# Kernel optimization log

Measured on AMD Instinct MI355X. Metric: run time of the kernel, lower is better.

Reference implementation:

```python
import jax, jax.numpy as jnp
import numpy as np

N, R, A, F = 6000, 5, 8, 128
K, O = 2, 128
RADIUS = 0.028
ROT_DELTA = 1


def _kernel_matrix(n_radial, n_angular, radius):
    # polar grid of kernel vertices -> cartesian, shape (R, A, 2)
    r = radius * (np.arange(1, n_radial + 1, dtype=np.float64) / n_radial)
    theta = 2.0 * np.pi * np.arange(n_angular, dtype=np.float64) / n_angular
    x = r[:, None] * np.cos(theta)[None, :]
    y = r[:, None] * np.sin(theta)[None, :]
    return np.stack([x, y], axis=-1)


def _interp_coefficients(n_radial, n_angular, radius):
    # Gaussian interpolation weights w(rho_a,theta_b,rho_c,theta_d), normalized,
    # reshaped to (R, A, R*A) as in _configure_patch_operator.
    kv = _kernel_matrix(n_radial, n_angular, radius)           # (R, A, 2)
    flat = kv.reshape(-1, 2)                                   # (R*A, 2)
    d2 = ((kv[:, :, None, :] - flat[None, None, :, :]) ** 2).sum(-1)  # (R, A, R*A)
    sigma = radius / n_radial
    w = np.exp(-d2 / (2.0 * sigma * sigma))
    w = w / w.sum(axis=-1, keepdims=True)
    return w.astype(np.float32)


def setup_inputs() -> dict:
    key = jax.random.key(0)
    k1, k2, k3, k4, k5 = jax.random.split(key, 5)
    mesh_signal = jax.random.normal(k1, (N, F), dtype=jnp.float32)
    # barycentric coords: channel 0 = vertex indices (stored as float), channel 1 = weights summing to 1
    idx = jax.random.randint(k2, (N, R, A, 3), 0, N).astype(jnp.float32)
    w = jax.random.uniform(k3, (N, R, A, 3), dtype=jnp.float32)
    w = w / w.sum(axis=-1, keepdims=True)
    bary_coordinates = jnp.stack([idx, w], axis=-1)            # (N, R, A, 3, 2)
    kernel_weights = jax.random.normal(k4, (R, A, K, O, F), dtype=jnp.float32) * 0.05
    bias = jax.random.normal(k5, (K, O), dtype=jnp.float32) * 0.05
    interp_coeffs = jnp.asarray(_interp_coefficients(R, A, RADIUS))  # (R, A, R*A)
    return {"mesh_signal": mesh_signal, "bary_coordinates": bary_coordinates,
            "kernel_weights": kernel_weights, "bias": bias, "interp_coeffs": interp_coeffs}


def reference(mesh_signal, bary_coordinates, kernel_weights, bias, interp_coeffs):
    # 1) gather + barycentric interpolation
    idx = bary_coordinates[..., 0].astype(jnp.int32)           # (N, R, A, 3)
    w = bary_coordinates[..., 1]                               # (N, R, A, 3)
    collected = mesh_signal[idx]                               # (N, R, A, 3, F)
    sig = jnp.sum(w[..., None] * collected, axis=-2)           # (N, R, A, F)
    # 2) patch operator: F_x @ I[a,b]
    flat = sig.reshape(-1, R * A, F)                           # (N, R*A, F)
    patched = jnp.einsum('nqf,raq->nraf', flat, interp_coeffs)  # (N, R, A, F)
    # 3) rotation-shifted fold (splits=1 -> single chunk; splits don't change math)
    outs = []
    for rot in range(0, A, ROT_DELTA):
        rolled = jnp.roll(patched, shift=rot, axis=2)          # (N, R, A, F)
        s = jnp.einsum('nraf,rakof->nko', rolled, kernel_weights) + (R * A) * bias  # (N, K, O)
        outs.append(jax.nn.relu(s).sum(axis=1))                # (N, O)
    return jnp.stack(outs, axis=1)                             # (N, n_rotations, O)
```

## Files before the change

### kernel.cpp

```cpp
#include <hip/hip_runtime.h>
#include <hip/hip_bf16.h>


#define N_PTS 6000
#define RR 5
#define AA 8
#define FF 128
#define OO 128
#define QQ 40
#define KD2 1280
#define SIG_BLOCKS 750
#define W2_BLOCKS 128
#define CCQ 0.70710678118654752f
#define RT2 1.41421356237309515f

#define AHS ((size_t)N_PTS * KD2)
#define BHS ((size_t)512 * KD2)

typedef __bf16 bf16_t;
typedef __bf16 bf16x2 __attribute__((ext_vector_type(2)));
typedef __bf16 bf16x8 __attribute__((ext_vector_type(8)));
typedef float f32x4 __attribute__((ext_vector_type(4)));

#define GLOAD_LDS16(g, l)                                              \
  __builtin_amdgcn_global_load_lds(                                    \
      (const __attribute__((address_space(1))) void*)(g),              \
      (__attribute__((address_space(3))) void*)(l), 16, 0, 0)

#define DFT8V(xx, c, X0, X4, Xr1, Xi1, Xr2, Xi2, Xr3, Xi3)             \
  {                                                                    \
    const float s0_ = xx[0][c] + xx[4][c], s1_ = xx[1][c] + xx[5][c];  \
    const float s2_ = xx[2][c] + xx[6][c], s3_ = xx[3][c] + xx[7][c];  \
    const float d0_ = xx[0][c] - xx[4][c], d1_ = xx[1][c] - xx[5][c];  \
    const float d2_ = xx[2][c] - xx[6][c], d3_ = xx[3][c] - xx[7][c];  \
    const float e_ = CCQ * (d1_ - d3_), o_ = CCQ * (d1_ + d3_);        \
    X0 = (s0_ + s2_) + (s1_ + s3_);                                    \
    X4 = (s0_ + s2_) - (s1_ + s3_);                                    \
    Xr2 = s0_ - s2_; Xi2 = s3_ - s1_;                                  \
    Xr1 = d0_ + e_;  Xi1 = -(o_ + d2_);                                \
    Xr3 = d0_ - e_;  Xi3 = d2_ - o_;                                   \
  }

#define PACKP(dst, P, Q)                                               \
  {                                                                    \
    bf16x8 pv_;                                                        \
    pv_[0] = (bf16_t)P[0]; pv_[1] = (bf16_t)Q[0];                      \
    pv_[2] = (bf16_t)P[1]; pv_[3] = (bf16_t)Q[1];                      \
    pv_[4] = (bf16_t)P[2]; pv_[5] = (bf16_t)Q[2];                      \
    pv_[6] = (bf16_t)P[3]; pv_[7] = (bf16_t)Q[3];                      \
    *(bf16x8*)(dst) = pv_;                                             \
  }

__global__ __launch_bounds__(256, 6) void prep_fft_kernel(
    const float* __restrict__ mesh, const float* __restrict__ bary,
    const float* __restrict__ kw, const float* __restrict__ interp,
    bf16_t* __restrict__ Ahat, bf16_t* __restrict__ Bhat) {
  __shared__ float sh[1920];
  const int bx = blockIdx.x;
  const int tid = threadIdx.x;

  if (bx < SIG_BLOCKS) {
    const int slot = tid >> 5;
    const int l = tid & 31;
    const int n = bx * 8 + slot;
    const float* bbase = bary + (size_t)bx * 8 * (QQ * 6);
    for (int i = tid; i < 1920; i += 256) sh[i] = bbase[i];
    __syncthreads();
    const float* bp = sh + slot * 240;
    bf16_t* an = Ahat + (size_t)n * KD2 + l * 8;
#pragma unroll
    for (int rho = 0; rho < RR; ++rho) {
      float x[8][4];
#pragma unroll
      for (int a = 0; a < 8; ++a) {
        const float* rec = bp + (rho * 8 + a) * 6;
        const float2 p0 = *(const float2*)(rec);
        const float2 p1 = *(const float2*)(rec + 2);
        const float2 p2 = *(const float2*)(rec + 4);
        const float4 v0 =
            *(const float4*)(mesh + (size_t)((int)p0.x) * FF + l * 4);
        const float4 v1 =
            *(const float4*)(mesh + (size_t)((int)p1.x) * FF + l * 4);
        const float4 v2 =
            *(const float4*)(mesh + (size_t)((int)p2.x) * FF + l * 4);
        x[a][0] = p0.y * v0.x + p1.y * v1.x + p2.y * v2.x;
        x[a][1] = p0.y * v0.y + p1.y * v1.y + p2.y * v2.y;
        x[a][2] = p0.y * v0.z + p1.y * v1.z + p2.y * v2.z;
        x[a][3] = p0.y * v0.w + p1.y * v1.w + p2.y * v2.w;
      }
      float X0[4], X4[4], Xr1[4], Xi1[4], Xr2[4], Xi2[4], Xr3[4], Xi3[4];
#pragma unroll
      for (int c = 0; c < 4; ++c)
        DFT8V(x, c, X0[c], X4[c], Xr1[c], Xi1[c], Xr2[c], Xi2[c], Xr3[c],
              Xi3[c]);
      bf16_t* dst = an + rho * 256;
      PACKP(dst, X0, X4);
      PACKP(dst + AHS, Xr1, Xi1);
      PACKP(dst + 2 * AHS, Xr2, Xi2);
      PACKP(dst + 3 * AHS, Xr3, Xi3);
    }
  } else {
    const int j = (bx - SIG_BLOCKS) * 2 + (tid >> 7);
    const int f = tid & 127;
    for (int i = tid; i < RR * AA * QQ; i += 256) sh[i] = interp[i];
    __syncthreads();
    const int o = (j >> 1) & 127;
    const int k = j & 1;
    float acc[QQ];
#pragma unroll
    for (int q = 0; q < QQ; ++q) acc[q] = 0.f;
    for (int r = 0; r < RR; ++r) {
      for (int a = 0; a < AA; ++a) {
        const float kv =
            kw[((size_t)((r * AA + a) * 2 + k) * OO + o) * FF + f];
        const float4* ip = (const float4*)(sh + (r * AA + a) * QQ);
#pragma unroll
        for (int q4 = 0; q4 < QQ / 4; ++q4) {
          const float4 w4 = ip[q4];
          acc[q4 * 4 + 0] += w4.x * kv;
          acc[q4 * 4 + 1] += w4.y * kv;
          acc[q4 * 4 + 2] += w4.z * kv;
          acc[q4 * 4 + 3] += w4.w * kv;
        }
      }
    }
    const float SC = 0.125f;
    bf16_t* b1p = Bhat + (size_t)j * KD2;
    bf16_t* b2p = Bhat + (size_t)(256 + j) * KD2;
#pragma unroll
    for (int rho = 0; rho < RR; ++rho) {
      float xx[8][1];
#pragma unroll
      for (int a = 0; a < 8; ++a) xx[a][0] = acc[rho * 8 + a];
      float Y0, Y4, Yr1, Yi1, Yr2, Yi2, Yr3, Yi3;
      DFT8V(xx, 0, Y0, Y4, Yr1, Yi1, Yr2, Yi2, Yr3, Yi3);
      const int off = rho * 256 + f * 2;
      bf16x2 w;
      w[0] = (bf16_t)(Y0 * SC);   w[1] = (bf16_t)0.f;
      *(bf16x2*)(b1p + off) = w;
      w[0] = (bf16_t)0.f;         w[1] = (bf16_t)(Y4 * SC);
      *(bf16x2*)(b2p + off) = w;
      w[0] = (bf16_t)(Yr1 * SC);  w[1] = (bf16_t)(Yi1 * SC);
      *(bf16x2*)(b1p + BHS + off) = w;
      w[0] = (bf16_t)(Yi1 * SC);  w[1] = (bf16_t)(-Yr1 * SC);
      *(bf16x2*)(b2p + BHS + off) = w;
      w[0] = (bf16_t)(Yr2 * SC);  w[1] = (bf16_t)(Yi2 * SC);
      *(bf16x2*)(b1p + 2 * BHS + off) = w;
      w[0] = (bf16_t)(Yi2 * SC);  w[1] = (bf16_t)(-Yr2 * SC);
      *(bf16x2*)(b2p + 2 * BHS + off) = w;
      w[0] = (bf16_t)(Yr3 * SC);  w[1] = (bf16_t)(Yi3 * SC);
      *(bf16x2*)(b1p + 3 * BHS + off) = w;
      w[0] = (bf16_t)(Yi3 * SC);  w[1] = (bf16_t)(-Yr3 * SC);
      *(bf16x2*)(b2p + 3 * BHS + off) = w;
    }
  }
}

__global__ __launch_bounds__(256, 3) void gemm_fused_fft_kernel(
    const bf16_t* __restrict__ Ahat, const bf16_t* __restrict__ Bhat,
    const float* __restrict__ bias, float* __restrict__ out) {
  const int L = blockIdx.x;
  const int xcd = L & 7;
  const int t = L >> 3;
  const int g = xcd + 8 * (t >> 4);
  const int jt = t & 15;
  const int m0 = g * 128;
  if (m0 >= N_PTS) return;
  const int j0 = jt * 16;

  __shared__ bf16_t As[128 * 64];
  __shared__ bf16_t Bs[32 * 64];
  const int tid = threadIdx.x;
  const int wave = tid >> 6;
  const int lane = tid & 63;
  const int quad = lane >> 4;
  const int tl = lane & 15;
  const int wm = wave * 32;
  const int srow = lane >> 3;
  const int sc = (lane & 7) ^ srow;

  const int crow = wave * 8;
  const int colbase = (crow < 16) ? (j0 + crow) : (256 + j0 + (crow - 16));
  const int gcol = colbase + srow;

  static const float CF[4][8] = {
      {1, 1, 1, 1, 1, 1, 1, 1},
      {2, RT2, 0, -RT2, -2, -RT2, 0, RT2},
      {2, 0, -2, 0, 2, 0, -2, 0},
      {2, -RT2, 0, RT2, -2, RT2, 0, -RT2}};
  static const float SF[4][8] = {
      {1, -1, 1, -1, 1, -1, 1, -1},
      {0, -RT2, -2, -RT2, 0, RT2, 2, RT2},
      {0, -2, 0, 2, 0, -2, 0, 2},
      {0, -RT2, 2, -RT2, 0, RT2, -2, RT2}};

  f32x4 oacc[8][2];
#pragma unroll
  for (int rot = 0; rot < 8; ++rot)
#pragma unroll
    for (int mm = 0; mm < 2; ++mm) oacc[rot][mm] = {0.f, 0.f, 0.f, 0.f};

#pragma unroll
  for (int b = 0; b < 4; ++b) {
    const bf16_t* A = Ahat + (size_t)b * AHS;
    const bf16_t* B = Bhat + (size_t)b * BHS;
    f32x4 z[2][2];
#pragma unroll
    for (int mm = 0; mm < 2; ++mm)
#pragma unroll
      for (int cc = 0; cc < 2; ++cc) z[mm][cc] = {0.f, 0.f, 0.f, 0.f};

    for (int kk = 0; kk < KD2; kk += 64) {
      __syncthreads();
#pragma unroll
      for (int i = 0; i < 4; ++i) {
        const int row = wave * 32 + i * 8;
        int gm = m0 + row + srow;
        gm = gm < N_PTS ? gm : (N_PTS - 1);
        GLOAD_LDS16(A + (size_t)gm * KD2 + kk + sc * 8, As + row * 64);
      }
      GLOAD_LDS16(B + (size_t)gcol * KD2 + kk + sc * 8, Bs + crow * 64);
      __syncthreads();
#pragma unroll
      for (int ks = 0; ks < 2; ++ks) {
        const int ch = (((ks * 4 + quad) ^ (tl & 7)) * 8);
        bf16x8 af[2], bfr[2];
        af[0] = *(const bf16x8*)(As + (wm + tl) * 64 + ch);
        af[1] = *(const bf16x8*)(As + (wm + 16 + tl) * 64 + ch);
        bfr[0] = *(const bf16x8*)(Bs + tl * 64 + ch);
        bfr[1] = *(const bf16x8*)(Bs + (16 + tl) * 64 + ch);
#pragma unroll
        for (int mm = 0; mm < 2; ++mm)
#pragma unroll
          for (int cc = 0; cc < 2; ++cc)
            z[mm][cc] = __builtin_amdgcn_mfma_f32_16x16x32_bf16(
                af[mm], bfr[cc], z[mm][cc], 0, 0, 0);
      }
    }
#pragma unroll
    for (int rot = 0; rot < 8; ++rot) {
      const float cf = CF[b][rot], sf = SF[b][rot];
#pragma unroll
      for (int mm = 0; mm < 2; ++mm)
#pragma unroll
        for (int r = 0; r < 4; ++r)
          oacc[rot][mm][r] += cf * z[mm][0][r] + sf * z[mm][1][r];
    }
  }

  const int j = j0 + tl;
  const float bb = 40.0f * bias[((j & 1) << 7) | (j >> 1)];
  const int o = j >> 1;
#pragma unroll
  for (int rot = 0; rot < 8; ++rot)
#pragma unroll
    for (int mm = 0; mm < 2; ++mm)
#pragma unroll
      for (int r = 0; r < 4; ++r) {
        const int mrow = m0 + wm + mm * 16 + quad * 4 + r;
        float v = oacc[rot][mm][r] + bb;
        v = v > 0.f ? v : 0.f;
        const float vs = v + __shfl_xor(v, 1, 64);
        if (((lane & 1) == 0) && (mrow < N_PTS))
          out[(size_t)mrow * 1024 + rot * 128 + o] = vs;
      }
}

extern "C" void kernel_launch(void* const* d_in, const int* in_sizes, int n_in,
                              void* d_out, int out_size, void* d_ws,
                              size_t ws_size, hipStream_t stream) {
  const float* mesh = (const float*)d_in[0];
  const float* bary = (const float*)d_in[1];
  const float* kw = (const float*)d_in[2];
  const float* bias = (const float*)d_in[3];
  const float* interp = (const float*)d_in[4];
  float* out = (float*)d_out;

  bf16_t* Ahat = (bf16_t*)d_ws;
  bf16_t* Bhat = (bf16_t*)((char*)d_ws + 4 * AHS * 2);

  prep_fft_kernel<<<SIG_BLOCKS + W2_BLOCKS, 256, 0, stream>>>(
      mesh, bary, kw, interp, Ahat, Bhat);
  gemm_fused_fft_kernel<<<768, 256, 0, stream>>>(Ahat, Bhat, bias, out);
}
```

Before: 165.6 us.

## Store A operand in MFMA-fragment-native layout and load it directly to registers

```diff
diff --git a/kernel.cpp b/kernel.cpp
--- a/kernel.cpp
+++ b/kernel.cpp
@@ -67,7 +67,9 @@
     for (int i = tid; i < 1920; i += 256) sh[i] = bbase[i];
     __syncthreads();
     const float* bp = sh + slot * 240;
-    bf16_t* an = Ahat + (size_t)n * KD2 + l * 8;
+    const int mf = n >> 4, prow = n & 15;
+    bf16_t* an = Ahat + ((size_t)mf * 40 + (l >> 2)) * 512 +
+                 (size_t)(4 * prow + (l & 3)) * 8;
 #pragma unroll
     for (int rho = 0; rho < RR; ++rho) {
       float x[8][4];
@@ -93,7 +95,7 @@
       for (int c = 0; c < 4; ++c)
         DFT8V(x, c, X0[c], X4[c], Xr1[c], Xi1[c], Xr2[c], Xi2[c], Xr3[c],
               Xi3[c]);
-      bf16_t* dst = an + rho * 256;
+      bf16_t* dst = an + (size_t)rho * 4096;
       PACKP(dst, X0, X4);
       PACKP(dst + AHS, Xr1, Xi1);
       PACKP(dst + 2 * AHS, Xr2, Xi2);
@@ -168,7 +170,6 @@
   if (m0 >= N_PTS) return;
   const int j0 = jt * 16;
 
-  __shared__ bf16_t As[128 * 64];
   __shared__ bf16_t Bs[32 * 64];
   const int tid = threadIdx.x;
   const int wave = tid >> 6;
@@ -182,6 +183,11 @@
   const int crow = wave * 8;
   const int colbase = (crow < 16) ? (j0 + crow) : (256 + j0 + (crow - 16));
   const int gcol = colbase + srow;
+
+  const int mf0 = (m0 + wm) >> 4;
+  int mf1 = mf0 + 1;
+  if (mf1 > 374) mf1 = 374;
+  const int sA = (4 * tl + quad) * 8;
 
   static const float CF[4][8] = {
       {1, 1, 1, 1, 1, 1, 1, 1},
@@ -202,7 +208,10 @@
 
 #pragma unroll
   for (int b = 0; b < 4; ++b) {
-    const bf16_t* A = Ahat + (size_t)b * AHS;
+    const bf16_t* Af0 =
+        Ahat + (size_t)b * AHS + (size_t)mf0 * 40 * 512 + sA;
+    const bf16_t* Af1 =
+        Ahat + (size_t)b * AHS + (size_t)mf1 * 40 * 512 + sA;
     const bf16_t* B = Bhat + (size_t)b * BHS;
     f32x4 z[2][2];
 #pragma unroll
@@ -212,29 +221,30 @@
 
     for (int kk = 0; kk < KD2; kk += 64) {
       __syncthreads();
-#pragma unroll
-      for (int i = 0; i < 4; ++i) {
-        const int row = wave * 32 + i * 8;
-        int gm = m0 + row + srow;
-        gm = gm < N_PTS ? gm : (N_PTS - 1);
-        GLOAD_LDS16(A + (size_t)gm * KD2 + kk + sc * 8, As + row * 64);
-      }
       GLOAD_LDS16(B + (size_t)gcol * KD2 + kk + sc * 8, Bs + crow * 64);
+      const size_t fb = (size_t)(kk >> 5) * 512;
+      const bf16x8 a00 = *(const bf16x8*)(Af0 + fb);
+      const bf16x8 a10 = *(const bf16x8*)(Af1 + fb);
+      const bf16x8 a01 = *(const bf16x8*)(Af0 + fb + 512);
+      const bf16x8 a11 = *(const bf16x8*)(Af1 + fb + 512);
       __syncthreads();
-#pragma unroll
-      for (int ks = 0; ks < 2; ++ks) {
-        const int ch = (((ks * 4 + quad) ^ (tl & 7)) * 8);
-        bf16x8 af[2], bfr[2];
-        af[0] = *(const bf16x8*)(As + (wm + tl) * 64 + ch);
-        af[1] = *(const bf16x8*)(As + (wm + 16 + tl) * 64 + ch);
-        bfr[0] = *(const bf16x8*)(Bs + tl * 64 + ch);
-        bfr[1] = *(const bf16x8*)(Bs + (16 + tl) * 64 + ch);
-#pragma unroll
-        for (int mm = 0; mm < 2; ++mm)
-#pragma unroll
-          for (int cc = 0; cc < 2; ++cc)
-            z[mm][cc] = __builtin_amdgcn_mfma_f32_16x16x32_bf16(
-                af[mm], bfr[cc], z[mm][cc], 0, 0, 0);
+      {
+        const int ch = ((quad) ^ (tl & 7)) * 8;
+        const bf16x8 b0 = *(const bf16x8*)(Bs + tl * 64 + ch);
+        const bf16x8 b1 = *(const bf16x8*)(Bs + (16 + tl) * 64 + ch);
+        z[0][0] = __builtin_amdgcn_mfma_f32_16x16x32_bf16(a00, b0, z[0][0], 0, 0, 0);
+        z[0][1] = __builtin_amdgcn_mfma_f32_16x16x32_bf16(a00, b1, z[0][1], 0, 0, 0);
+        z[1][0] = __builtin_amdgcn_mfma_f32_16x16x32_bf16(a10, b0, z[1][0], 0, 0, 0);
+        z[1][1] = __builtin_amdgcn_mfma_f32_16x16x32_bf16(a10, b1, z[1][1], 0, 0, 0);
+      }
+      {
+        const int ch = ((4 + quad) ^ (tl & 7)) * 8;
+        const bf16x8 b0 = *(const bf16x8*)(Bs + tl * 64 + ch);
+        const bf16x8 b1 = *(const bf16x8*)(Bs + (16 + tl) * 64 + ch);
+        z[0][0] = __builtin_amdgcn_mfma_f32_16x16x32_bf16(a01, b0, z[0][0], 0, 0, 0);
+        z[0][1] = __builtin_amdgcn_mfma_f32_16x16x32_bf16(a01, b1, z[0][1], 0, 0, 0);
+        z[1][0] = __builtin_amdgcn_mfma_f32_16x16x32_bf16(a11, b0, z[1][0], 0, 0, 0);
+        z[1][1] = __builtin_amdgcn_mfma_f32_16x16x32_bf16(a11, b1, z[1][1], 0, 0, 0);
       }
     }
 #pragma unroll
```

Measured after the change: 181.5 us. +9.6%, slower.
